# Kernel optimization log

Measured on AMD Instinct MI355X. Metric: run time of the kernel, lower is better.

Reference implementation:

```python
import jax, jax.numpy as jnp
import numpy as np

EMBED = 1024
HEADS = 16
HEAD_DIM = EMBED // HEADS


def setup_inputs() -> dict:
    key = jax.random.key(0)
    ks = jax.random.split(key, 11)
    N, S = 2, 2048
    scale = 1.0 / np.sqrt(EMBED)
    inp = {
        "values": jax.random.normal(ks[0], (N, S, EMBED), jnp.float32),
        "keys": jax.random.normal(ks[1], (N, S, EMBED), jnp.float32),
        "queries": jax.random.normal(ks[2], (N, S, EMBED), jnp.float32),
        "W_v": jax.random.normal(ks[3], (EMBED, EMBED), jnp.float32) * scale,
        "b_v": jnp.zeros((EMBED,), jnp.float32),
        "W_k": jax.random.normal(ks[4], (EMBED, EMBED), jnp.float32) * scale,
        "b_k": jnp.zeros((EMBED,), jnp.float32),
        "W_q": jax.random.normal(ks[5], (EMBED, EMBED), jnp.float32) * scale,
        "b_q": jnp.zeros((EMBED,), jnp.float32),
        "W_o": jax.random.normal(ks[6], (EMBED, EMBED), jnp.float32) * scale,
        "b_o": jnp.zeros((EMBED,), jnp.float32),
    }
    return inp


def reference(values, keys, queries, W_v, b_v, W_k, b_k, W_q, b_q, W_o, b_o):
    N, q_len, _ = queries.shape
    # linear projections then split heads: [N, S, H, Dh]
    v = (values @ W_v.T + b_v).reshape(N, -1, HEADS, HEAD_DIM)
    k = (keys @ W_k.T + b_k).reshape(N, -1, HEADS, HEAD_DIM)
    q = (queries @ W_q.T + b_q).reshape(N, q_len, HEADS, HEAD_DIM)
    # raw scores [N, H, Q, K]
    energy = jnp.einsum("nqhd,nkhd->nhqk", q, k)
    attention = jax.nn.softmax(energy / np.sqrt(HEAD_DIM), axis=-1)
    out = jnp.einsum("nhql,nlhd->nqhd", attention, v).reshape(N, q_len, EMBED)
    return out @ W_o.T + b_o
```

## Files before the change

### kernel.cpp

```cpp
#include <hip/hip_runtime.h>
#include <hip/hip_bf16.h>


typedef short bf16x8 __attribute__((ext_vector_type(8)));
typedef short bf16x4 __attribute__((ext_vector_type(4)));
typedef float f32x4 __attribute__((ext_vector_type(4)));
typedef float f32x16 __attribute__((ext_vector_type(16)));
typedef unsigned u32x2 __attribute__((ext_vector_type(2)));
typedef unsigned u32x4 __attribute__((ext_vector_type(4)));

constexpr int S = 2048;
constexpr int E = 1024;
constexpr int H = 16;
constexpr int D = 64;
constexpr int M = 2 * S;
#define QSCALE 0.18033688011112042f

static __device__ __forceinline__ short f2bf_rne(float x) {
  unsigned u = __builtin_bit_cast(unsigned, x);
  u += 0x7fff + ((u >> 16) & 1);
  return (short)(u >> 16);
}
static __device__ __forceinline__ bf16x8 cvt8(float4 a, float4 b) {
  bf16x8 t;
  t[0] = f2bf_rne(a.x); t[1] = f2bf_rne(a.y);
  t[2] = f2bf_rne(a.z); t[3] = f2bf_rne(a.w);
  t[4] = f2bf_rne(b.x); t[5] = f2bf_rne(b.y);
  t[6] = f2bf_rne(b.z); t[7] = f2bf_rne(b.w);
  return t;
}
static __device__ __forceinline__ float fast_exp2(float x) {
#if __has_builtin(__builtin_amdgcn_exp2f)
  return __builtin_amdgcn_exp2f(x);
#else
  return __expf(0.69314718055994531f * x);
#endif
}
static __device__ __forceinline__ unsigned cvtpk(float a, float b) {
  unsigned r;
  asm("v_cvt_pk_bf16_f32 %0, %1, %2" : "=v"(r) : "v"(a), "v"(b));
  return r;
}
static __device__ __forceinline__ void plswap(unsigned& a, unsigned& b) {
#if __has_builtin(__builtin_amdgcn_permlane32_swap)
  u32x2 t = __builtin_amdgcn_permlane32_swap(a, b, false, false);
  a = t[0]; b = t[1];
#else
  asm("v_permlane32_swap_b32 %0, %1" : "+v"(a), "+v"(b));
#endif
}

static __device__ __forceinline__ void gl_lds16(const short* g, short* l) {
  __builtin_amdgcn_global_load_lds(
      (const __attribute__((address_space(1))) void*)g,
      (__attribute__((address_space(3))) void*)l, 16, 0, 0);
}


__global__ __launch_bounds__(256) void cast_all(
    const float* __restrict__ qs, const float* __restrict__ ks,
    const float* __restrict__ vsrc, const float* __restrict__ wq,
    const float* __restrict__ wk, const float* __restrict__ wv,
    const float* __restrict__ wo, short* __restrict__ qbf,
    short* __restrict__ kbf, short* __restrict__ vbf, short* __restrict__ wqb,
    short* __restrict__ wkb, short* __restrict__ wvb, short* __restrict__ wob) {
  const float* s;
  short* d;
  switch (blockIdx.y) {
    case 0: s = qs; d = qbf; break;
    case 1: s = ks; d = kbf; break;
    case 2: s = vsrc; d = vbf; break;
    case 3: if (blockIdx.x >= 512) return; s = wq; d = wqb; break;
    case 4: if (blockIdx.x >= 512) return; s = wk; d = wkb; break;
    case 5: if (blockIdx.x >= 512) return; s = wv; d = wvb; break;
    default: if (blockIdx.x >= 512) return; s = wo; d = wob; break;
  }
  size_t i = ((size_t)blockIdx.x * 256 + threadIdx.x) * 8;
  *(bf16x8*)&d[i] = cvt8(*(const float4*)&s[i], *(const float4*)&s[i + 4]);
}

__global__ __launch_bounds__(256) void qk_gemm(
    const short* __restrict__ qbf, const short* __restrict__ kbf,
    const short* __restrict__ wqb, const short* __restrict__ wkb,
    const float* __restrict__ bq, const float* __restrict__ bk,
    short* __restrict__ qb, short* __restrict__ kb) {
  __shared__ __align__(16) short as[128 * 32];
  __shared__ __align__(16) short bs[128 * 32];
  const int tid = threadIdx.x;
  const int lane = tid & 63, w = tid >> 6;
  const int l15 = lane & 15, quad = lane >> 4;
  const int wm = w & 1, wn = w >> 1;

  const int b = blockIdx.x;
  const int c = b & 7, r = b >> 3;
  const int bn = r & 7;
  const int t = c * 8 + (r >> 3);
  const int z = t >> 5, bm = t & 31;

  const short* A = z ? kbf : qbf;
  const short* Bw = z ? wkb : wqb;
  const float* bias = z ? bk : bq;

  const short* agp[2];
  const short* bgp[2];
  int ldsb[2];
#pragma unroll
  for (int cc = 0; cc < 2; ++cc) {
    int seg = w * 2 + cc;
    int p = seg * 8 + (lane >> 3), kc = lane & 7;
    int l = kc ^ (p & 7);
    int row = 2 * p + (l >> 2), col = (l & 3) * 8;
    ldsb[cc] = seg * 512;
    agp[cc] = &A[(size_t)(bm * 128 + row) * E + col];
    bgp[cc] = &Bw[(size_t)(bn * 128 + row) * E + col];
  }

  f32x4 acc[4][4] = {};
  for (int k0 = 0; k0 < E; k0 += 32) {
    __syncthreads();
#pragma unroll
    for (int cc = 0; cc < 2; ++cc) {
      gl_lds16(agp[cc] + k0, &as[ldsb[cc]]);
      gl_lds16(bgp[cc] + k0, &bs[ldsb[cc]]);
    }
    __syncthreads();

    bf16x8 af[4], bf[4];
#pragma unroll
    for (int tt = 0; tt < 4; ++tt) {
      int ra = wm * 64 + tt * 16 + l15;
      int pa2 = ra >> 1, la = (ra & 1) * 4 + quad, ka = la ^ (pa2 & 7);
      af[tt] = *(bf16x8*)&as[pa2 * 64 + ka * 8];
      int rb = wn * 64 + tt * 16 + l15;
      int pb2 = rb >> 1, lb = (rb & 1) * 4 + quad, kb2 = lb ^ (pb2 & 7);
      bf[tt] = *(bf16x8*)&bs[pb2 * 64 + kb2 * 8];
    }
#pragma unroll
    for (int mt = 0; mt < 4; ++mt)
#pragma unroll
      for (int nt = 0; nt < 4; ++nt)
        acc[mt][nt] = __builtin_amdgcn_mfma_f32_16x16x32_bf16(
            af[mt], bf[nt], acc[mt][nt], 0, 0, 0);
  }

#pragma unroll
  for (int mt = 0; mt < 4; ++mt)
#pragma unroll
    for (int nt = 0; nt < 4; ++nt)
#pragma unroll
      for (int rr = 0; rr < 4; ++rr) {
        int row = bm * 128 + wm * 64 + mt * 16 + quad * 4 + rr;
        int col = bn * 128 + wn * 64 + nt * 16 + l15;
        float v = acc[mt][nt][rr] + bias[col];
        int n = row >> 11, s = row & 2047, h = col >> 6, d = col & 63;
        if (z == 0) {
          qb[(((size_t)(n * H + h) * S) + s) * D + d] = f2bf_rne(v * QSCALE);
        } else {
          kb[(((size_t)(n * H + h) * S) + s) * D + d] = f2bf_rne(v);
        }
      }
}

template <int MODE>
__global__ __launch_bounds__(256) void gemm64(const short* __restrict__ A,
                                              const short* __restrict__ Bw,
                                              const float* __restrict__ bias,
                                              void* __restrict__ outp) {
  __shared__ __align__(16) short as[64 * 32];
  __shared__ __align__(16) short bs[128 * 32];
  const int tid = threadIdx.x;
  const int lane = tid & 63, w = tid >> 6;
  const int l15 = lane & 15, quad = lane >> 4;
  const int wm = w & 1, wn = w >> 1;

  const int b = blockIdx.x;
  const int c = b & 7, r = b >> 3;
  const int bn = r & 7;
  const int bm = c * 8 + (r >> 3);

  const short* agp;
  int aldsb;
  {
    int seg = w;
    int p = seg * 8 + (lane >> 3), kc = lane & 7;
    int l = kc ^ (p & 7);
    int row = 2 * p + (l >> 2), col = (l & 3) * 8;
    aldsb = seg * 512;
    agp = &A[(size_t)(bm * 64 + row) * E + col];
  }
  const short* bgp[2];
  int bldsb[2];
#pragma unroll
  for (int cc = 0; cc < 2; ++cc) {
    int seg = w * 2 + cc;
    int p = seg * 8 + (lane >> 3), kc = lane & 7;
    int l = kc ^ (p & 7);
    int row = 2 * p + (l >> 2), col = (l & 3) * 8;
    bldsb[cc] = seg * 512;
    bgp[cc] = &Bw[(size_t)(bn * 128 + row) * E + col];
  }

  f32x4 acc[2][4] = {};
  for (int k0 = 0; k0 < E; k0 += 32) {
    __syncthreads();
    gl_lds16(agp + k0, &as[aldsb]);
#pragma unroll
    for (int cc = 0; cc < 2; ++cc) gl_lds16(bgp[cc] + k0, &bs[bldsb[cc]]);
    __syncthreads();

    bf16x8 af[2], bf[4];
#pragma unroll
    for (int tt = 0; tt < 2; ++tt) {
      int ra = wm * 32 + tt * 16 + l15;
      int pa2 = ra >> 1, la = (ra & 1) * 4 + quad, ka = la ^ (pa2 & 7);
      af[tt] = *(bf16x8*)&as[pa2 * 64 + ka * 8];
    }
#pragma unroll
    for (int tt = 0; tt < 4; ++tt) {
      int rb = wn * 64 + tt * 16 + l15;
      int pb2 = rb >> 1, lb = (rb & 1) * 4 + quad, kb2 = lb ^ (pb2 & 7);
      bf[tt] = *(bf16x8*)&bs[pb2 * 64 + kb2 * 8];
    }
#pragma unroll
    for (int mt = 0; mt < 2; ++mt)
#pragma unroll
      for (int nt = 0; nt < 4; ++nt)
        acc[mt][nt] = __builtin_amdgcn_mfma_f32_16x16x32_bf16(
            af[mt], bf[nt], acc[mt][nt], 0, 0, 0);
  }

#pragma unroll
  for (int mt = 0; mt < 2; ++mt)
#pragma unroll
    for (int nt = 0; nt < 4; ++nt)
#pragma unroll
      for (int rr = 0; rr < 4; ++rr) {
        int row = bm * 64 + wm * 32 + mt * 16 + quad * 4 + rr;
        int col = bn * 128 + wn * 64 + nt * 16 + l15;
        float v = acc[mt][nt][rr] + bias[col];
        if (MODE == 0) {
          int n = row >> 11, s = row & 2047, h = col >> 6, d = col & 63;
          ((short*)outp)[(((size_t)(n * H + h) * D) + d) * S + s] =
              f2bf_rne(v);
        } else {
          ((float*)outp)[(size_t)row * E + col] = v;
        }
      }
}

__global__ __launch_bounds__(512) void attn_kernel(const short* __restrict__ q,
                                                   const short* __restrict__ k,
                                                   const short* __restrict__ vt,
                                                   short* __restrict__ ctx) {
  __shared__ __align__(16) short smem[128 * 72 + 64 * 136];
  short* ks = smem;
  short* vs = smem + 128 * 72;
  float* mrg = (float*)smem;

  const int tid = threadIdx.x;
  const int lane = tid & 63, wv = tid >> 6;
  const int l31 = lane & 31, h = lane >> 5;
  const int qg = wv & 3, kh = wv >> 2;

  const int bid = blockIdx.y * gridDim.x + blockIdx.x;
  const int c = bid & 7, r = bid >> 3;
  const int qt = r & 15;
  const int hz = c * 4 + (r >> 4);
  const int hh = hz & 15, nn = hz >> 4;

  const size_t base = (size_t)(nn * H + hh) * S * D;
  const int q0 = qt * 128 + qg * 32;

  bf16x8 qf[4];
#pragma unroll
  for (int kd = 0; kd < 4; ++kd)
    qf[kd] = *(const bf16x8*)&q[base + (size_t)(q0 + l31) * D + kd * 16 + h * 8];

  f32x16 o[2] = {};
  float lsum = 0.f;

  bf16x8 pk[2], pv[2];
  auto loadKV = [&](int j0) {
#pragma unroll
    for (int cc = 0; cc < 2; ++cc) {
      int ch = cc * 512 + tid;
      int kr = ch >> 3, kc = (ch & 7) * 8;
      pk[cc] = *(const bf16x8*)&k[base + (size_t)(j0 + kr) * D + kc];
      int vr = ch >> 4, vc = (ch & 15) * 8;
      pv[cc] = *(const bf16x8*)&vt[base + (size_t)vr * S + j0 + vc];
    }
  };

  loadKV(0);
  for (int j0 = 0; j0 < S; j0 += 128) {
    __syncthreads();
#pragma unroll
    for (int cc = 0; cc < 2; ++cc) {
      int ch = cc * 512 + tid;
      int kr = ch >> 3, kc = (ch & 7) * 8;
      *(bf16x8*)&ks[kr * 72 + kc] = pk[cc];
      int vr = ch >> 4, vc = (ch & 15) * 8;
      *(bf16x8*)&vs[vr * 136 + vc] = pv[cc];
    }
    __syncthreads();
    if (j0 + 128 < S) loadKV(j0 + 128);

    f32x16 sc[2] = {};
#pragma unroll
    for (int c2 = 0; c2 < 2; ++c2)
#pragma unroll
      for (int kd = 0; kd < 4; ++kd) {
        bf16x8 kf = *(bf16x8*)&ks[(kh * 64 + c2 * 32 + l31) * 72 +
                                  kd * 16 + h * 8];
        sc[c2] = __builtin_amdgcn_mfma_f32_32x32x16_bf16(kf, qf[kd], sc[c2],
                                                         0, 0, 0);
      }

    bf16x8 pa[4];
#pragma unroll
    for (int c2 = 0; c2 < 2; ++c2) {
      float pe[16];
#pragma unroll
      for (int rr = 0; rr < 16; ++rr) {
        float p = fast_exp2(sc[c2][rr]);
        lsum += p;
        pe[rr] = p;
      }
#pragma unroll
      for (int kk = 0; kk < 2; ++kk) {
        unsigned A0 = cvtpk(pe[8 * kk + 0], pe[8 * kk + 1]);
        unsigned A1 = cvtpk(pe[8 * kk + 2], pe[8 * kk + 3]);
        unsigned B0 = cvtpk(pe[8 * kk + 4], pe[8 * kk + 5]);
        unsigned B1 = cvtpk(pe[8 * kk + 6], pe[8 * kk + 7]);
        plswap(A0, B0);
        plswap(A1, B1);
        u32x4 t;
        t[0] = A0; t[1] = A1; t[2] = B0; t[3] = B1;
        pa[c2 * 2 + kk] = __builtin_bit_cast(bf16x8, t);
      }
    }

#pragma unroll
    for (int ks2 = 0; ks2 < 4; ++ks2)
#pragma unroll
      for (int dc = 0; dc < 2; ++dc) {
        bf16x8 vf = *(bf16x8*)&vs[(dc * 32 + l31) * 136 + kh * 64 +
                                  ks2 * 16 + h * 8];
        o[dc] = __builtin_amdgcn_mfma_f32_32x32x16_bf16(pa[ks2], vf, o[dc],
                                                        0, 0, 0);
      }
  }

  lsum += __shfl_xor(lsum, 32);

  __syncthreads();
  if (kh == 1) {
#pragma unroll
    for (int rr = 0; rr < 16; ++rr) {
      int crow = (rr & 3) + 8 * (rr >> 2) + 4 * h;
#pragma unroll
      for (int dc = 0; dc < 2; ++dc)
        mrg[qg * 2080 + crow * 64 + dc * 32 + l31] = o[dc][rr];
    }
    if (h == 0) mrg[qg * 2080 + 2048 + l31] = lsum;
  }
  __syncthreads();
  if (kh == 0) {
    lsum += mrg[qg * 2080 + 2048 + l31];
    float invq = 1.0f / lsum;
#pragma unroll
    for (int rr = 0; rr < 16; ++rr) {
      int crow = (rr & 3) + 8 * (rr >> 2) + 4 * h;
      float inv = __shfl(invq, crow);
      int row = q0 + crow;
#pragma unroll
      for (int dc = 0; dc < 2; ++dc) {
        float val = o[dc][rr] + mrg[qg * 2080 + crow * 64 + dc * 32 + l31];
        ctx[((size_t)(nn * S + row)) * E + hh * D + dc * 32 + l31] =
            f2bf_rne(val * inv);
      }
    }
  }
}

extern "C" void kernel_launch(void* const* d_in, const int* in_sizes, int n_in,
                              void* d_out, int out_size, void* d_ws,
                              size_t ws_size, hipStream_t stream) {
  const float* values  = (const float*)d_in[0];
  const float* keys    = (const float*)d_in[1];
  const float* queries = (const float*)d_in[2];
  const float* b_v = (const float*)d_in[4];
  const float* b_k = (const float*)d_in[6];
  const float* b_q = (const float*)d_in[8];
  const float* W_v = (const float*)d_in[3];
  const float* W_k = (const float*)d_in[5];
  const float* W_q = (const float*)d_in[7];
  const float* W_o = (const float*)d_in[9];
  const float* b_o = (const float*)d_in[10];

  const size_t X = (size_t)M * E;
  const size_t W = (size_t)E * E;

  short* qbf = (short*)d_out;
  short* qb  = (short*)d_out + X;
  short* kbf = (short*)d_ws;
  short* vbf = kbf + X;
  short* vtb = vbf + X;
  short* wqb = vtb + X;
  short* wkb = wqb + W;
  short* wvb = wkb + W;
  short* wob = wvb + W;
  short* ctx = kbf;
  short* kb  = vbf;

  cast_all<<<dim3(2048, 7), 256, 0, stream>>>(queries, keys, values, W_q, W_k,
                                              W_v, W_o, qbf, kbf, vbf, wqb,
                                              wkb, wvb, wob);
  gemm64<0><<<512, 256, 0, stream>>>(vbf, wvb, b_v, vtb);
  qk_gemm<<<512, 256, 0, stream>>>(qbf, kbf, wqb, wkb, b_q, b_k, qb, kb);
  attn_kernel<<<dim3(16, 32), 512, 0, stream>>>(qb, kb, vtb, ctx);
  gemm64<1><<<512, 256, 0, stream>>>(ctx, wob, b_o, d_out);
}
```

Before: 220.2 us.

## Restructure attention to 256 query rows per block with double-buffered K/V

The attention kernel no longer splits the key range across two wave groups that merge through shared memory. Each of the 8 waves now owns 32 query rows over all keys, so a block covers 256 queries and the grid is halved. K/V tiles are double-buffered in LDS, cutting one barrier per iteration, and s_setprio is raised around the MFMA sections. This raises K/V reuse and drops the merge step, but halves the block count (256 blocks on 256 CUs), which may hurt occupancy and latency hiding.

```diff
diff --git a/kernel.cpp b/kernel.cpp
--- a/kernel.cpp
+++ b/kernel.cpp
@@ -252,24 +252,21 @@
                                                    const short* __restrict__ k,
                                                    const short* __restrict__ vt,
                                                    short* __restrict__ ctx) {
-  __shared__ __align__(16) short smem[128 * 72 + 64 * 136];
-  short* ks = smem;
-  short* vs = smem + 128 * 72;
-  float* mrg = (float*)smem;
+  __shared__ __align__(16) short ksb[2][128 * 72];
+  __shared__ __align__(16) short vsb[2][64 * 136];
 
   const int tid = threadIdx.x;
   const int lane = tid & 63, wv = tid >> 6;
   const int l31 = lane & 31, h = lane >> 5;
-  const int qg = wv & 3, kh = wv >> 2;
 
   const int bid = blockIdx.y * gridDim.x + blockIdx.x;
   const int c = bid & 7, r = bid >> 3;
-  const int qt = r & 15;
-  const int hz = c * 4 + (r >> 4);
+  const int qt = r & 7;
+  const int hz = c * 4 + (r >> 3);
   const int hh = hz & 15, nn = hz >> 4;
 
   const size_t base = (size_t)(nn * H + hh) * S * D;
-  const int q0 = qt * 128 + qg * 32;
+  const int q0 = qt * 256 + wv * 32;
 
   bf16x8 qf[4];
 #pragma unroll
@@ -290,95 +287,95 @@
       pv[cc] = *(const bf16x8*)&vt[base + (size_t)vr * S + j0 + vc];
     }
   };
-
-  loadKV(0);
-  for (int j0 = 0; j0 < S; j0 += 128) {
-    __syncthreads();
+  auto storeKV = [&](int bufi) {
 #pragma unroll
     for (int cc = 0; cc < 2; ++cc) {
       int ch = cc * 512 + tid;
       int kr = ch >> 3, kc = (ch & 7) * 8;
-      *(bf16x8*)&ks[kr * 72 + kc] = pk[cc];
+      *(bf16x8*)&ksb[bufi][kr * 72 + kc] = pk[cc];
       int vr = ch >> 4, vc = (ch & 15) * 8;
-      *(bf16x8*)&vs[vr * 136 + vc] = pv[cc];
+      *(bf16x8*)&vsb[bufi][vr * 136 + vc] = pv[cc];
+    }
+  };
+
+  loadKV(0);
+  storeKV(0);
+  loadKV(128);
+  __syncthreads();
+
+  for (int t = 0; t < 16; ++t) {
+    const int cur = t & 1;
+    if (t + 1 < 16) storeKV(cur ^ 1);
+    if (t + 2 < 16) loadKV((t + 2) * 128);
+    const short* ks = ksb[cur];
+    const short* vs = vsb[cur];
+
+#pragma unroll
+    for (int half = 0; half < 2; ++half) {
+      f32x16 sc[2] = {};
+      __builtin_amdgcn_s_setprio(1);
+#pragma unroll
+      for (int c2 = 0; c2 < 2; ++c2)
+#pragma unroll
+        for (int kd = 0; kd < 4; ++kd) {
+          bf16x8 kf = *(bf16x8*)&ks[(half * 64 + c2 * 32 + l31) * 72 +
+                                    kd * 16 + h * 8];
+          sc[c2] = __builtin_amdgcn_mfma_f32_32x32x16_bf16(kf, qf[kd], sc[c2],
+                                                           0, 0, 0);
+        }
+      __builtin_amdgcn_s_setprio(0);
+
+      bf16x8 pa[4];
+#pragma unroll
+      for (int c2 = 0; c2 < 2; ++c2) {
+        float pe[16];
+#pragma unroll
+        for (int rr = 0; rr < 16; ++rr) {
+          float p = fast_exp2(sc[c2][rr]);
+          lsum += p;
+          pe[rr] = p;
+        }
+#pragma unroll
+        for (int kk = 0; kk < 2; ++kk) {
+          unsigned A0 = cvtpk(pe[8 * kk + 0], pe[8 * kk + 1]);
+          unsigned A1 = cvtpk(pe[8 * kk + 2], pe[8 * kk + 3]);
+          unsigned B0 = cvtpk(pe[8 * kk + 4], pe[8 * kk + 5]);
+          unsigned B1 = cvtpk(pe[8 * kk + 6], pe[8 * kk + 7]);
+          plswap(A0, B0);
+          plswap(A1, B1);
+          u32x4 tt;
+          tt[0] = A0; tt[1] = A1; tt[2] = B0; tt[3] = B1;
+          pa[c2 * 2 + kk] = __builtin_bit_cast(bf16x8, tt);
+        }
+      }
+
+      __builtin_amdgcn_s_setprio(1);
+#pragma unroll
+      for (int ks2 = 0; ks2 < 4; ++ks2)
+#pragma unroll
+        for (int dc = 0; dc < 2; ++dc) {
+          bf16x8 vf = *(bf16x8*)&vs[(dc * 32 + l31) * 136 + half * 64 +
+                                    ks2 * 16 + h * 8];
+          o[dc] = __builtin_amdgcn_mfma_f32_32x32x16_bf16(pa[ks2], vf, o[dc],
+                                                          0, 0, 0);
+        }
+      __builtin_amdgcn_s_setprio(0);
     }
     __syncthreads();
-    if (j0 + 128 < S) loadKV(j0 + 128);
-
-    f32x16 sc[2] = {};
-#pragma unroll
-    for (int c2 = 0; c2 < 2; ++c2)
-#pragma unroll
-      for (int kd = 0; kd < 4; ++kd) {
-        bf16x8 kf = *(bf16x8*)&ks[(kh * 64 + c2 * 32 + l31) * 72 +
-                                  kd * 16 + h * 8];
-        sc[c2] = __builtin_amdgcn_mfma_f32_32x32x16_bf16(kf, qf[kd], sc[c2],
-                                                         0, 0, 0);
-      }
-
-    bf16x8 pa[4];
-#pragma unroll
-    for (int c2 = 0; c2 < 2; ++c2) {
-      float pe[16];
-#pragma unroll
-      for (int rr = 0; rr < 16; ++rr) {
-        float p = fast_exp2(sc[c2][rr]);
-        lsum += p;
-        pe[rr] = p;
-      }
-#pragma unroll
-      for (int kk = 0; kk < 2; ++kk) {
-        unsigned A0 = cvtpk(pe[8 * kk + 0], pe[8 * kk + 1]);
-        unsigned A1 = cvtpk(pe[8 * kk + 2], pe[8 * kk + 3]);
-        unsigned B0 = cvtpk(pe[8 * kk + 4], pe[8 * kk + 5]);
-        unsigned B1 = cvtpk(pe[8 * kk + 6], pe[8 * kk + 7]);
-        plswap(A0, B0);
-        plswap(A1, B1);
-        u32x4 t;
-        t[0] = A0; t[1] = A1; t[2] = B0; t[3] = B1;
-        pa[c2 * 2 + kk] = __builtin_bit_cast(bf16x8, t);
-      }
-    }
-
-#pragma unroll
-    for (int ks2 = 0; ks2 < 4; ++ks2)
-#pragma unroll
-      for (int dc = 0; dc < 2; ++dc) {
-        bf16x8 vf = *(bf16x8*)&vs[(dc * 32 + l31) * 136 + kh * 64 +
-                                  ks2 * 16 + h * 8];
-        o[dc] = __builtin_amdgcn_mfma_f32_32x32x16_bf16(pa[ks2], vf, o[dc],
-                                                        0, 0, 0);
-      }
   }
 
   lsum += __shfl_xor(lsum, 32);
-
-  __syncthreads();
-  if (kh == 1) {
-#pragma unroll
-    for (int rr = 0; rr < 16; ++rr) {
-      int crow = (rr & 3) + 8 * (rr >> 2) + 4 * h;
-#pragma unroll
-      for (int dc = 0; dc < 2; ++dc)
-        mrg[qg * 2080 + crow * 64 + dc * 32 + l31] = o[dc][rr];
-    }
-    if (h == 0) mrg[qg * 2080 + 2048 + l31] = lsum;
-  }
-  __syncthreads();
-  if (kh == 0) {
-    lsum += mrg[qg * 2080 + 2048 + l31];
-    float invq = 1.0f / lsum;
-#pragma unroll
-    for (int rr = 0; rr < 16; ++rr) {
-      int crow = (rr & 3) + 8 * (rr >> 2) + 4 * h;
-      float inv = __shfl(invq, crow);
-      int row = q0 + crow;
-#pragma unroll
-      for (int dc = 0; dc < 2; ++dc) {
-        float val = o[dc][rr] + mrg[qg * 2080 + crow * 64 + dc * 32 + l31];
-        ctx[((size_t)(nn * S + row)) * E + hh * D + dc * 32 + l31] =
-            f2bf_rne(val * inv);
-      }
+  float invq = 1.0f / lsum;
+
+#pragma unroll
+  for (int rr = 0; rr < 16; ++rr) {
+    int crow = (rr & 3) + 8 * (rr >> 2) + 4 * h;
+    float inv = __shfl(invq, crow);
+    int row = q0 + crow;
+#pragma unroll
+    for (int dc = 0; dc < 2; ++dc) {
+      ctx[((size_t)(nn * S + row)) * E + hh * D + dc * 32 + l31] =
+          f2bf_rne(o[dc][rr] * inv);
     }
   }
 }
@@ -418,6 +415,6 @@
                                               wkb, wvb, wob);
   gemm64<0><<<512, 256, 0, stream>>>(vbf, wvb, b_v, vtb);
   qk_gemm<<<512, 256, 0, stream>>>(qbf, kbf, wqb, wkb, b_q, b_k, qb, kb);
-  attn_kernel<<<dim3(16, 32), 512, 0, stream>>>(qb, kb, vtb, ctx);
+  attn_kernel<<<dim3(8, 32), 512, 0, stream>>>(qb, kb, vtb, ctx);
   gemm64<1><<<512, 256, 0, stream>>>(ctx, wob, b_o, d_out);
 }
```

New measurement: 211.5 us. 1.04x faster.
